# Kernel tuning notes

Hardware: AMD Instinct MI355X
Metric: run time of the kernel (lower is better)

## Reference

```python
import jax, jax.numpy as jnp
import numpy as np

B, N, X, Y, W1, W2, D = 2, 6, 8, 8, 8, 8, 128
H, DH = 4, 32
L = X * Y          # number of windows
QT = N * W1 * W2   # tokens per window
EPS = 1e-5


def _ln(x, g, b):
    m = x.mean(-1, keepdims=True)
    v = ((x - m) ** 2).mean(-1, keepdims=True)
    return (x - m) * jax.lax.rsqrt(v + EPS) * g + b


def _win(t):
    # b n x y w1 w2 d -> b (x y) (n w1 w2) d
    return t.transpose(0, 2, 3, 1, 4, 5, 6).reshape(B, L, QT, D)


def setup_inputs() -> dict:
    key = jax.random.key(0)
    ks = jax.random.split(key, 12)
    s = 0.02
    inp = {
        'q': jax.random.normal(ks[0], (B, N, X, Y, W1, W2, D), jnp.float32),
        'k': jax.random.normal(ks[1], (B, N, X, Y, W1, W2, D), jnp.float32),
        'v': jax.random.normal(ks[2], (B, N, X, Y, W1, W2, D), jnp.float32),
        'skip': jax.random.normal(ks[3], (B, X, Y, W1, W2, D), jnp.float32),
        'gq': jnp.ones((D,), jnp.float32), 'betq': jnp.zeros((D,), jnp.float32),
        'gk': jnp.ones((D,), jnp.float32), 'betk': jnp.zeros((D,), jnp.float32),
        'gv': jnp.ones((D,), jnp.float32), 'betv': jnp.zeros((D,), jnp.float32),
        'wq': jax.random.normal(ks[4], (D, H * DH), jnp.float32) * s,
        'bq': jnp.zeros((H * DH,), jnp.float32),
        'wk': jax.random.normal(ks[5], (D, H * DH), jnp.float32) * s,
        'bk': jnp.zeros((H * DH,), jnp.float32),
        'wv': jax.random.normal(ks[6], (D, H * DH), jnp.float32) * s,
        'bv': jnp.zeros((H * DH,), jnp.float32),
        'wp': jax.random.normal(ks[7], (H * DH, D), jnp.float32) * s,
        'bp': jnp.zeros((D,), jnp.float32),
    }
    return inp


def reference(q, k, v, skip, gq, betq, gk, betk, gv, betv,
              wq, bq, wk, bk, wv, bv, wp, bp):
    scale = DH ** -0.5
    qw, kw, vw = _win(q), _win(k), _win(v)
    # LayerNorm + Linear QKV, split heads: (b, l, T, h, dh)
    qh = (_ln(qw, gq, betq) @ wq + bq).reshape(B, L, QT, H, DH)
    kh = (_ln(kw, gk, betk) @ wk + bk).reshape(B, L, QT, H, DH)
    vh = (_ln(vw, gv, betv) @ wv + bv).reshape(B, L, QT, H, DH)
    dot = scale * jnp.einsum('blqhd,blkhd->bhlqk', qh, kh)
    att = jax.nn.softmax(dot, axis=-1)
    a = jnp.einsum('bhlqk,blkhd->blqhd', att, vh).reshape(B, L, QT, H * DH)
    # b (x y) (n w1 w2) d -> b n x y w1 w2 d
    a = a.reshape(B, X, Y, N, W1, W2, H * DH).transpose(0, 3, 1, 2, 4, 5, 6)
    z = a @ wp + bp
    z = z.mean(1)  # average over views
    return z + skip
```

## Files before the change

### kernel.cpp

```cpp
#include <hip/hip_runtime.h>


typedef unsigned short u16;
typedef __bf16 bf16x8 __attribute__((ext_vector_type(8)));
typedef __bf16 bf16x4 __attribute__((ext_vector_type(4)));
typedef float  f32x16 __attribute__((ext_vector_type(16)));
typedef unsigned short u16x8 __attribute__((ext_vector_type(8)));
typedef unsigned short u16x4 __attribute__((ext_vector_type(4)));

union U8 { u16x8 u; bf16x8 b; u16x4 h[2]; };

#if __has_builtin(__builtin_amdgcn_exp2f)
#define EXP2(x) __builtin_amdgcn_exp2f(x)
#else
#define EXP2(x) exp2f(x)
#endif

__device__ __forceinline__ f32x16 mfma_bf16(bf16x8 a, bf16x8 b, f32x16 c){
  return __builtin_amdgcn_mfma_f32_32x32x16_bf16(a, b, c, 0, 0, 0);
}


__global__ __launch_bounds__(512) void k_prep(
    const float* __restrict__ wq, const float* __restrict__ bq,
    const float* __restrict__ gq, const float* __restrict__ betq,
    const float* __restrict__ wk, const float* __restrict__ bk,
    const float* __restrict__ gk, const float* __restrict__ betk,
    const float* __restrict__ wv, const float* __restrict__ bv,
    const float* __restrict__ gv, const float* __restrict__ betv,
    const float* __restrict__ wp,
    u16* __restrict__ wqT, u16* __restrict__ wkT, u16* __restrict__ wvT, u16* __restrict__ wpT,
    float* __restrict__ bq2, float* __restrict__ bk2, float* __restrict__ bv2,
    float* __restrict__ uq2, float* __restrict__ uk2, float* __restrict__ uv2)
{
  __shared__ float wls[128*33];
  __shared__ float gls[128], bls[128];
  __shared__ float redb[128], redu[128];
  const float ALPHA_Q = 0.17677669529663687f * 1.4426950408889634f;
  int bid = blockIdx.x, tid = threadIdx.x;
  int wsel = bid >> 2, chunk = bid & 3;
  const float *w, *bb, *g, *bet; u16* wT; float *b2, *u2; float alpha;
  if (wsel == 0){ w=wq; bb=bq; g=gq; bet=betq; wT=wqT; b2=bq2; u2=uq2; alpha=ALPHA_Q; }
  else if (wsel == 1){ w=wk; bb=bk; g=gk; bet=betk; wT=wkT; b2=bk2; u2=uk2; alpha=1.f; }
  else if (wsel == 2){ w=wv; bb=bv; g=gv; bet=betv; wT=wvT; b2=bv2; u2=uv2; alpha=1.f; }
  else { w=wp; bb=nullptr; g=nullptr; bet=nullptr; wT=wpT; b2=nullptr; u2=nullptr; alpha=1.f; }

  if (tid < 128){
    gls[tid] = g ? g[tid] : 1.f;
    bls[tid] = bet ? bet[tid] : 0.f;
  }
  const float4* w4 = (const float4*)w;
  #pragma unroll
  for (int i = 0; i < 2; i++){
    int idx = tid + i*512;
    int row = idx >> 3, f4c = idx & 7;
    float4 x = w4[row*32 + chunk*8 + f4c];
    wls[row*33 + f4c*4 + 0] = x.x;
    wls[row*33 + f4c*4 + 1] = x.y;
    wls[row*33 + f4c*4 + 2] = x.z;
    wls[row*33 + f4c*4 + 3] = x.w;
  }
  __syncthreads();
  if (tid < 128){
    int nl = tid >> 2, qp = tid & 3;
    float sb = 0.f, su = 0.f;
    alignas(16) __bf16 tmp[32];
    #pragma unroll
    for (int kk = 0; kk < 32; kk++){
      int k2 = qp*32 + kk;
      float wv_ = wls[k2*33 + nl];
      float gv_ = gls[k2];
      sb += bls[k2] * wv_;
      su += gv_ * wv_;
      tmp[kk] = (__bf16)(wv_ * gv_ * alpha);
    }
    int n = chunk*32 + nl;
    #pragma unroll
    for (int j = 0; j < 4; j++)
      *(bf16x8*)(wT + n*128 + qp*32 + j*8) = *(bf16x8*)&tmp[j*8];
    redb[tid] = sb; redu[tid] = su;
  }
  __syncthreads();
  if (tid < 128){
    int nl = tid >> 2, qp = tid & 3;
    if (qp == 0 && bb){
      int n = chunk*32 + nl;
      float s = bb[n] + redb[tid] + redb[tid+1] + redb[tid+2] + redb[tid+3];
      float u = redu[tid] + redu[tid+1] + redu[tid+2] + redu[tid+3];
      b2[n] = s * alpha;
      u2[n] = u * alpha;
    }
  }
}

__global__ __launch_bounds__(256) void k_lnproj(
    const float* __restrict__ qg, const float* __restrict__ kg, const float* __restrict__ vg,
    const u16* __restrict__ wqT, const u16* __restrict__ wkT, const u16* __restrict__ wvT,
    const float* __restrict__ bq2, const float* __restrict__ bk2, const float* __restrict__ bv2,
    const float* __restrict__ uq2, const float* __restrict__ uk2, const float* __restrict__ uv2,
    u16* __restrict__ qh, u16* __restrict__ kh, u16* __restrict__ vh)
{
  __shared__ alignas(16) u16 Abf[64*136];
  __shared__ float s1s[64], s2s[64];
  int bid = blockIdx.x, tid = threadIdx.x;
  int which = bid % 3;
  int t = bid / 3;
  int n = t % 6, bl = t / 6;
  const float* src; const u16* wT; const float *b2, *u2; u16* dstb;
  if (which == 0){ src=qg; wT=wqT; b2=bq2; u2=uq2; dstb=qh; }
  else if (which == 1){ src=kg; wT=wkT; b2=bk2; u2=uk2; dstb=kh; }
  else { src=vg; wT=wvT; b2=bv2; u2=uv2; dstb=vh; }
  int b = bl >> 6, l = bl & 63;
  const float4* s4 = (const float4*)(src + (size_t)((b*6 + n)*64 + l)*64*128);
  int row = tid >> 2, j = tid & 3;
  float s1 = 0.f, s2 = 0.f;
  #pragma unroll
  for (int i = 0; i < 8; i++){
    float4 xv = s4[row*32 + i*4 + j];
    s1 += xv.x + xv.y + xv.z + xv.w;
    s2 += xv.x*xv.x + xv.y*xv.y + xv.z*xv.z + xv.w*xv.w;
    bf16x4 pk;
    pk[0] = (__bf16)xv.x; pk[1] = (__bf16)xv.y;
    pk[2] = (__bf16)xv.z; pk[3] = (__bf16)xv.w;
    *(bf16x4*)&Abf[row*136 + (i*4 + j)*4] = pk;
  }
  s1 += __shfl_xor(s1, 1, 64); s1 += __shfl_xor(s1, 2, 64);
  s2 += __shfl_xor(s2, 1, 64); s2 += __shfl_xor(s2, 2, 64);
  if (j == 0){
    float m = s1 * (1.f/128.f);
    float r = rsqrtf(s2 * (1.f/128.f) - m*m + 1e-5f);
    s1s[row] = r;
    s2s[row] = r * m;
  }
  __syncthreads();
  int wave = tid >> 6, lane = tid & 63, lm = lane & 31, lh = lane >> 5;
  bf16x8 bfr[8];
  const u16* wrow = wT + (32*wave + lm)*128 + lh*8;
  #pragma unroll
  for (int ks = 0; ks < 8; ks++) bfr[ks] = *(const bf16x8*)(wrow + ks*16);
  f32x16 acc0, acc1;
  #pragma unroll
  for (int r = 0; r < 16; r++){ acc0[r]=0.f; acc1[r]=0.f; }
  #pragma unroll
  for (int ks = 0; ks < 8; ks++){
    bf16x8 a0 = *(const bf16x8*)&Abf[lm*136       + ks*16 + lh*8];
    bf16x8 a1 = *(const bf16x8*)&Abf[(32+lm)*136  + ks*16 + lh*8];
    acc0 = mfma_bf16(a0, bfr[ks], acc0);
    acc1 = mfma_bf16(a1, bfr[ks], acc1);
  }
  int col = 32*wave + lm;
  float u2c = u2[col], bc = b2[col];
  u16* dst = dstb + ((size_t)(bl*4 + wave)*384 + n*64)*32 + lm;
  #pragma unroll
  for (int r = 0; r < 16; r++){
    int row0 = (r&3) + 8*(r>>2) + 4*lh;
    float y0 = s1s[row0]     * acc0[r] - s2s[row0]     * u2c + bc;
    float y1 = s1s[row0+32]  * acc1[r] - s2s[row0+32]  * u2c + bc;
    *(__bf16*)&dst[(size_t)row0*32]      = (__bf16)y0;
    *(__bf16*)&dst[(size_t)(32+row0)*32] = (__bf16)y1;
  }
}

__global__ __launch_bounds__(384) void k_attn(
    const u16* __restrict__ qh, const u16* __restrict__ kh, const u16* __restrict__ vh,
    u16* __restrict__ abar)
{
  __shared__ alignas(16) u16 vts[32*392];
  __shared__ float abar_s[64*32];
  int bid = blockIdx.x, tid = threadIdx.x;
  int h = bid & 3, bl = bid >> 2;
  const u16* qb = qh + (size_t)bid * (384*32);
  const u16* kb = kh + (size_t)bid * (384*32);
  const u16* vb = vh + (size_t)bid * (384*32);

  int wave = tid >> 6, lane = tid & 63, lm = lane & 31, lh = lane >> 5;
  int n = wave;

  const u16* qbase = qb + (size_t)(n*64 + lm)*32 + lh*8;
  bf16x8 qfA0 = *(const bf16x8*)(qbase);
  bf16x8 qfA1 = *(const bf16x8*)(qbase + 16);
  bf16x8 qfB0 = *(const bf16x8*)(qbase + 32*32);
  bf16x8 qfB1 = *(const bf16x8*)(qbase + 32*32 + 16);

  #pragma unroll
  for (int i = 0; i < 4; i++){
    int c = tid + i*384;
    int key = c >> 2, part = c & 3;
    int u = key & 31, tt = key >> 5;
    int a = u >> 2;
    int anew = (a & 4) | ((a & 1) << 1) | ((a >> 1) & 1);
    int pos = tt*32 + anew*4 + (u & 3);
    u16x8 vv = *(const u16x8*)(vb + key*32 + part*8);
    #pragma unroll
    for (int jj = 0; jj < 8; jj++) vts[(part*8 + jj)*392 + pos] = vv[jj];
  }
  for (int idx = tid; idx < 2048; idx += 384) abar_s[idx] = 0.f;
  __syncthreads();

  const u16* vrow = &vts[lm*392 + 8*lh];
  const u16* krow = kb + lm*32 + lh*8;

  bf16x8 ones;
  #pragma unroll
  for (int j = 0; j < 8; j++) ones[j] = (__bf16)1.0f;

  f32x16 oA, oB, slA, slB;
  #pragma unroll
  for (int r = 0; r < 16; r++){ oA[r]=0.f; oB[r]=0.f; slA[r]=0.f; slB[r]=0.f; }

  #pragma unroll
  for (int kt = 0; kt < 12; kt++){
    bf16x8 kf0 = *(const bf16x8*)(krow + kt*1024);
    bf16x8 kf1 = *(const bf16x8*)(krow + kt*1024 + 16);
    f32x16 sa, sb_;
    #pragma unroll
    for (int r = 0; r < 16; r++){ sa[r] = 0.f; sb_[r] = 0.f; }
    __builtin_amdgcn_s_setprio(1);
    sa  = mfma_bf16(kf0, qfA0, sa);
    sb_ = mfma_bf16(kf0, qfB0, sb_);
    sa  = mfma_bf16(kf1, qfA1, sa);
    sb_ = mfma_bf16(kf1, qfB1, sb_);
    __builtin_amdgcn_s_setprio(0);
    U8 v0, v1;
    v0.u = *(const u16x8*)(vrow + kt*32);
    v1.u = *(const u16x8*)(vrow + kt*32 + 16);
    U8 pA0, pA1, pB0, pB1;
    #pragma unroll
    for (int r = 0; r < 8; r++){
      pA0.b[r] = (__bf16)EXP2(sa[r]);
      pA1.b[r] = (__bf16)EXP2(sa[r+8]);
      pB0.b[r] = (__bf16)EXP2(sb_[r]);
      pB1.b[r] = (__bf16)EXP2(sb_[r+8]);
    }
    __builtin_amdgcn_s_setprio(1);
    oA  = mfma_bf16(pA0.b, v0.b, oA);
    oB  = mfma_bf16(pB0.b, v0.b, oB);
    slA = mfma_bf16(pA0.b, ones, slA);
    slB = mfma_bf16(pB0.b, ones, slB);
    oA  = mfma_bf16(pA1.b, v1.b, oA);
    oB  = mfma_bf16(pB1.b, v1.b, oB);
    slA = mfma_bf16(pA1.b, ones, slA);
    slB = mfma_bf16(pB1.b, ones, slB);
    __builtin_amdgcn_s_setprio(0);
  }

  #pragma unroll
  for (int r = 0; r < 16; r++){
    int q_l = (r&3) + 8*(r>>2) + 4*lh;
    float ia = (1.f/6.f) * __builtin_amdgcn_rcpf(slA[r]);
    float ib = (1.f/6.f) * __builtin_amdgcn_rcpf(slB[r]);
    atomicAdd(&abar_s[q_l*32 + lm], oA[r]*ia);
    atomicAdd(&abar_s[(32 + q_l)*32 + lm], oB[r]*ib);
  }
  __syncthreads();
  u16* ob = abar + (size_t)(bl*64)*128 + h*32;
  for (int idx = tid; idx < 2048; idx += 384){
    int w12 = idx >> 5, dh = idx & 31;
    *(__bf16*)&ob[(size_t)w12*128 + dh] = (__bf16)abar_s[idx];
  }
}

__global__ __launch_bounds__(256) void k_out(
    const u16* __restrict__ abar, const u16* __restrict__ wpT,
    const float* __restrict__ bp, const float* __restrict__ skip,
    float* __restrict__ out)
{
  __shared__ alignas(16) u16 Als[32*136];
  int tid = threadIdx.x;
  int R0 = blockIdx.x * 32;
  #pragma unroll
  for (int i = 0; i < 2; i++){
    int c = tid + i*256;
    int row = c >> 4, part = c & 15;
    *(u16x8*)&Als[row*136 + part*8] = *(const u16x8*)(abar + (size_t)(R0+row)*128 + part*8);
  }
  __syncthreads();
  int wave = tid >> 6, lane = tid & 63, lm = lane & 31, lh = lane >> 5;
  bf16x8 bfr[8];
  const u16* wrow = wpT + (32*wave + lm)*128 + lh*8;
  #pragma unroll
  for (int ks = 0; ks < 8; ks++) bfr[ks] = *(const bf16x8*)(wrow + ks*16);
  f32x16 acc;
  #pragma unroll
  for (int r = 0; r < 16; r++) acc[r] = 0.f;
  #pragma unroll
  for (int ks = 0; ks < 8; ks++){
    bf16x8 a0 = *(const bf16x8*)&Als[lm*136 + ks*16 + lh*8];
    acc = mfma_bf16(a0, bfr[ks], acc);
  }
  float bias = bp[32*wave + lm];
  #pragma unroll
  for (int r = 0; r < 16; r++){
    int row0 = (r&3) + 8*(r>>2) + 4*lh;
    size_t f0 = (size_t)(R0 + row0)*128 + 32*wave + lm;
    out[f0] = acc[r] + bias + skip[f0];
  }
}

extern "C" void kernel_launch(void* const* d_in, const int* in_sizes, int n_in,
                              void* d_out, int out_size, void* d_ws, size_t ws_size,
                              hipStream_t stream)
{
  const float* q    = (const float*)d_in[0];
  const float* k    = (const float*)d_in[1];
  const float* v    = (const float*)d_in[2];
  const float* skip = (const float*)d_in[3];
  const float* gq   = (const float*)d_in[4];
  const float* betq = (const float*)d_in[5];
  const float* gk   = (const float*)d_in[6];
  const float* betk = (const float*)d_in[7];
  const float* gv   = (const float*)d_in[8];
  const float* betv = (const float*)d_in[9];
  const float* wq   = (const float*)d_in[10];
  const float* bq   = (const float*)d_in[11];
  const float* wk   = (const float*)d_in[12];
  const float* bk   = (const float*)d_in[13];
  const float* wv   = (const float*)d_in[14];
  const float* bv   = (const float*)d_in[15];
  const float* wp   = (const float*)d_in[16];
  const float* bp   = (const float*)d_in[17];
  float* out = (float*)d_out;

  char* ws = (char*)d_ws;
  u16* wqT = (u16*)ws;
  u16* wkT = wqT + 16384;
  u16* wvT = wkT + 16384;
  u16* wpT = wvT + 16384;
  float* bq2 = (float*)(ws + 131072);
  float* bk2 = bq2 + 128;
  float* bv2 = bk2 + 128;
  float* uq2 = bv2 + 128;
  float* uk2 = uq2 + 128;
  float* uv2 = uk2 + 128;
  u16* qh = (u16*)(ws + 134144);
  u16* kh = qh + 6291456;
  u16* vh = kh + 6291456;
  u16* abar = vh + 6291456;

  k_prep  <<<16,   512, 0, stream>>>(wq,bq,gq,betq, wk,bk,gk,betk, wv,bv,gv,betv, wp,
                                     wqT,wkT,wvT,wpT, bq2,bk2,bv2, uq2,uk2,uv2);
  k_lnproj<<<2304, 256, 0, stream>>>(q,k,v, wqT,wkT,wvT, bq2,bk2,bv2, uq2,uk2,uv2, qh,kh,vh);
  k_attn  <<<512,  384, 0, stream>>>(qh,kh,vh, abar);
  k_out   <<<256,  256, 0, stream>>>(abar, wpT, bp, skip, out);
}
```

Before: 205.9 us.

## Fuse prep, LN-projection, attention and output kernels into one persistent kernel

Replaces the four separate launches (weight prep, LayerNorm+QKV projection, windowed attention, output projection) with one persistent kernel of 512 blocks. The stages are separated by a software grid barrier built on agent-scope atomics, and the barrier counters are reset in rotation. The projection stage is remapped so each 512-thread block runs two 256-thread slots over three passes. The aim is to remove inter-kernel launch gaps and tail effects. The cost is spin-wait barriers, a dependence on all blocks being co-resident, and idle waves in the attention and output stages.

```diff
diff --git a/kernel.cpp b/kernel.cpp
--- a/kernel.cpp
+++ b/kernel.cpp
@@ -20,280 +20,314 @@
   return __builtin_amdgcn_mfma_f32_32x32x16_bf16(a, b, c, 0, 0, 0);
 }
 
-
-__global__ __launch_bounds__(512) void k_prep(
+#define NBLK 512
+
+__device__ int g_bar[3];
+
+__device__ __forceinline__ void grid_sync(int idx){
+  __threadfence();
+  __syncthreads();
+  if (threadIdx.x == 0){
+    int prev = __hip_atomic_fetch_add(&g_bar[idx], 1, __ATOMIC_ACQ_REL,
+                                      __HIP_MEMORY_SCOPE_AGENT);
+    if (prev == NBLK - 1)
+      __hip_atomic_store(&g_bar[(idx+2)%3], 0, __ATOMIC_RELAXED,
+                         __HIP_MEMORY_SCOPE_AGENT);
+    while (__hip_atomic_load(&g_bar[idx], __ATOMIC_ACQUIRE,
+                             __HIP_MEMORY_SCOPE_AGENT) < NBLK)
+      __builtin_amdgcn_s_sleep(2);
+  }
+  __syncthreads();
+}
+
+
+__global__ __launch_bounds__(512, 4) void k_fused(
+    const float* __restrict__ q, const float* __restrict__ k,
+    const float* __restrict__ v, const float* __restrict__ skip,
+    const float* __restrict__ gq, const float* __restrict__ betq,
+    const float* __restrict__ gk, const float* __restrict__ betk,
+    const float* __restrict__ gv, const float* __restrict__ betv,
     const float* __restrict__ wq, const float* __restrict__ bq,
-    const float* __restrict__ gq, const float* __restrict__ betq,
     const float* __restrict__ wk, const float* __restrict__ bk,
-    const float* __restrict__ gk, const float* __restrict__ betk,
     const float* __restrict__ wv, const float* __restrict__ bv,
-    const float* __restrict__ gv, const float* __restrict__ betv,
-    const float* __restrict__ wp,
-    u16* __restrict__ wqT, u16* __restrict__ wkT, u16* __restrict__ wvT, u16* __restrict__ wpT,
+    const float* __restrict__ wp, const float* __restrict__ bp,
+    float* __restrict__ out,
+    u16* __restrict__ wqT, u16* __restrict__ wkT, u16* __restrict__ wvT,
+    u16* __restrict__ wpT,
     float* __restrict__ bq2, float* __restrict__ bk2, float* __restrict__ bv2,
-    float* __restrict__ uq2, float* __restrict__ uk2, float* __restrict__ uv2)
-{
-  __shared__ float wls[128*33];
-  __shared__ float gls[128], bls[128];
-  __shared__ float redb[128], redu[128];
-  const float ALPHA_Q = 0.17677669529663687f * 1.4426950408889634f;
-  int bid = blockIdx.x, tid = threadIdx.x;
-  int wsel = bid >> 2, chunk = bid & 3;
-  const float *w, *bb, *g, *bet; u16* wT; float *b2, *u2; float alpha;
-  if (wsel == 0){ w=wq; bb=bq; g=gq; bet=betq; wT=wqT; b2=bq2; u2=uq2; alpha=ALPHA_Q; }
-  else if (wsel == 1){ w=wk; bb=bk; g=gk; bet=betk; wT=wkT; b2=bk2; u2=uk2; alpha=1.f; }
-  else if (wsel == 2){ w=wv; bb=bv; g=gv; bet=betv; wT=wvT; b2=bv2; u2=uv2; alpha=1.f; }
-  else { w=wp; bb=nullptr; g=nullptr; bet=nullptr; wT=wpT; b2=nullptr; u2=nullptr; alpha=1.f; }
-
-  if (tid < 128){
-    gls[tid] = g ? g[tid] : 1.f;
-    bls[tid] = bet ? bet[tid] : 0.f;
-  }
-  const float4* w4 = (const float4*)w;
-  #pragma unroll
-  for (int i = 0; i < 2; i++){
-    int idx = tid + i*512;
-    int row = idx >> 3, f4c = idx & 7;
-    float4 x = w4[row*32 + chunk*8 + f4c];
-    wls[row*33 + f4c*4 + 0] = x.x;
-    wls[row*33 + f4c*4 + 1] = x.y;
-    wls[row*33 + f4c*4 + 2] = x.z;
-    wls[row*33 + f4c*4 + 3] = x.w;
-  }
-  __syncthreads();
-  if (tid < 128){
-    int nl = tid >> 2, qp = tid & 3;
-    float sb = 0.f, su = 0.f;
-    alignas(16) __bf16 tmp[32];
-    #pragma unroll
-    for (int kk = 0; kk < 32; kk++){
-      int k2 = qp*32 + kk;
-      float wv_ = wls[k2*33 + nl];
-      float gv_ = gls[k2];
-      sb += bls[k2] * wv_;
-      su += gv_ * wv_;
-      tmp[kk] = (__bf16)(wv_ * gv_ * alpha);
-    }
-    int n = chunk*32 + nl;
-    #pragma unroll
-    for (int j = 0; j < 4; j++)
-      *(bf16x8*)(wT + n*128 + qp*32 + j*8) = *(bf16x8*)&tmp[j*8];
-    redb[tid] = sb; redu[tid] = su;
-  }
-  __syncthreads();
-  if (tid < 128){
-    int nl = tid >> 2, qp = tid & 3;
-    if (qp == 0 && bb){
-      int n = chunk*32 + nl;
-      float s = bb[n] + redb[tid] + redb[tid+1] + redb[tid+2] + redb[tid+3];
-      float u = redu[tid] + redu[tid+1] + redu[tid+2] + redu[tid+3];
-      b2[n] = s * alpha;
-      u2[n] = u * alpha;
-    }
-  }
-}
-
-__global__ __launch_bounds__(256) void k_lnproj(
-    const float* __restrict__ qg, const float* __restrict__ kg, const float* __restrict__ vg,
-    const u16* __restrict__ wqT, const u16* __restrict__ wkT, const u16* __restrict__ wvT,
-    const float* __restrict__ bq2, const float* __restrict__ bk2, const float* __restrict__ bv2,
-    const float* __restrict__ uq2, const float* __restrict__ uk2, const float* __restrict__ uv2,
-    u16* __restrict__ qh, u16* __restrict__ kh, u16* __restrict__ vh)
-{
-  __shared__ alignas(16) u16 Abf[64*136];
-  __shared__ float s1s[64], s2s[64];
-  int bid = blockIdx.x, tid = threadIdx.x;
-  int which = bid % 3;
-  int t = bid / 3;
-  int n = t % 6, bl = t / 6;
-  const float* src; const u16* wT; const float *b2, *u2; u16* dstb;
-  if (which == 0){ src=qg; wT=wqT; b2=bq2; u2=uq2; dstb=qh; }
-  else if (which == 1){ src=kg; wT=wkT; b2=bk2; u2=uk2; dstb=kh; }
-  else { src=vg; wT=wvT; b2=bv2; u2=uv2; dstb=vh; }
-  int b = bl >> 6, l = bl & 63;
-  const float4* s4 = (const float4*)(src + (size_t)((b*6 + n)*64 + l)*64*128);
-  int row = tid >> 2, j = tid & 3;
-  float s1 = 0.f, s2 = 0.f;
-  #pragma unroll
-  for (int i = 0; i < 8; i++){
-    float4 xv = s4[row*32 + i*4 + j];
-    s1 += xv.x + xv.y + xv.z + xv.w;
-    s2 += xv.x*xv.x + xv.y*xv.y + xv.z*xv.z + xv.w*xv.w;
-    bf16x4 pk;
-    pk[0] = (__bf16)xv.x; pk[1] = (__bf16)xv.y;
-    pk[2] = (__bf16)xv.z; pk[3] = (__bf16)xv.w;
-    *(bf16x4*)&Abf[row*136 + (i*4 + j)*4] = pk;
-  }
-  s1 += __shfl_xor(s1, 1, 64); s1 += __shfl_xor(s1, 2, 64);
-  s2 += __shfl_xor(s2, 1, 64); s2 += __shfl_xor(s2, 2, 64);
-  if (j == 0){
-    float m = s1 * (1.f/128.f);
-    float r = rsqrtf(s2 * (1.f/128.f) - m*m + 1e-5f);
-    s1s[row] = r;
-    s2s[row] = r * m;
-  }
-  __syncthreads();
-  int wave = tid >> 6, lane = tid & 63, lm = lane & 31, lh = lane >> 5;
-  bf16x8 bfr[8];
-  const u16* wrow = wT + (32*wave + lm)*128 + lh*8;
-  #pragma unroll
-  for (int ks = 0; ks < 8; ks++) bfr[ks] = *(const bf16x8*)(wrow + ks*16);
-  f32x16 acc0, acc1;
-  #pragma unroll
-  for (int r = 0; r < 16; r++){ acc0[r]=0.f; acc1[r]=0.f; }
-  #pragma unroll
-  for (int ks = 0; ks < 8; ks++){
-    bf16x8 a0 = *(const bf16x8*)&Abf[lm*136       + ks*16 + lh*8];
-    bf16x8 a1 = *(const bf16x8*)&Abf[(32+lm)*136  + ks*16 + lh*8];
-    acc0 = mfma_bf16(a0, bfr[ks], acc0);
-    acc1 = mfma_bf16(a1, bfr[ks], acc1);
-  }
-  int col = 32*wave + lm;
-  float u2c = u2[col], bc = b2[col];
-  u16* dst = dstb + ((size_t)(bl*4 + wave)*384 + n*64)*32 + lm;
-  #pragma unroll
-  for (int r = 0; r < 16; r++){
-    int row0 = (r&3) + 8*(r>>2) + 4*lh;
-    float y0 = s1s[row0]     * acc0[r] - s2s[row0]     * u2c + bc;
-    float y1 = s1s[row0+32]  * acc1[r] - s2s[row0+32]  * u2c + bc;
-    *(__bf16*)&dst[(size_t)row0*32]      = (__bf16)y0;
-    *(__bf16*)&dst[(size_t)(32+row0)*32] = (__bf16)y1;
-  }
-}
-
-__global__ __launch_bounds__(384) void k_attn(
-    const u16* __restrict__ qh, const u16* __restrict__ kh, const u16* __restrict__ vh,
+    float* __restrict__ uq2, float* __restrict__ uk2, float* __restrict__ uv2,
+    u16* __restrict__ qh, u16* __restrict__ kh, u16* __restrict__ vh,
     u16* __restrict__ abar)
 {
-  __shared__ alignas(16) u16 vts[32*392];
-  __shared__ float abar_s[64*32];
-  int bid = blockIdx.x, tid = threadIdx.x;
-  int h = bid & 3, bl = bid >> 2;
-  const u16* qb = qh + (size_t)bid * (384*32);
-  const u16* kb = kh + (size_t)bid * (384*32);
-  const u16* vb = vh + (size_t)bid * (384*32);
-
-  int wave = tid >> 6, lane = tid & 63, lm = lane & 31, lh = lane >> 5;
-  int n = wave;
-
-  const u16* qbase = qb + (size_t)(n*64 + lm)*32 + lh*8;
-  bf16x8 qfA0 = *(const bf16x8*)(qbase);
-  bf16x8 qfA1 = *(const bf16x8*)(qbase + 16);
-  bf16x8 qfB0 = *(const bf16x8*)(qbase + 32*32);
-  bf16x8 qfB1 = *(const bf16x8*)(qbase + 32*32 + 16);
-
-  #pragma unroll
-  for (int i = 0; i < 4; i++){
-    int c = tid + i*384;
-    int key = c >> 2, part = c & 3;
-    int u = key & 31, tt = key >> 5;
-    int a = u >> 2;
-    int anew = (a & 4) | ((a & 1) << 1) | ((a >> 1) & 1);
-    int pos = tt*32 + anew*4 + (u & 3);
-    u16x8 vv = *(const u16x8*)(vb + key*32 + part*8);
+  __shared__ __align__(16) char smem[35840];
+  int tid = threadIdx.x;
+
+  if (blockIdx.x < 16){
+    float* wls  = (float*)smem;
+    float* gls  = (float*)(smem + 16896);
+    float* bls  = (float*)(smem + 17408);
+    float* redb = (float*)(smem + 17920);
+    float* redu = (float*)(smem + 18432);
+    const float ALPHA_Q = 0.17677669529663687f * 1.4426950408889634f;
+    int wsel = blockIdx.x >> 2, chunk = blockIdx.x & 3;
+    const float *w, *bb, *g, *bet; u16* wT; float *b2, *u2; float alpha;
+    if (wsel == 0){ w=wq; bb=bq; g=gq; bet=betq; wT=wqT; b2=bq2; u2=uq2; alpha=ALPHA_Q; }
+    else if (wsel == 1){ w=wk; bb=bk; g=gk; bet=betk; wT=wkT; b2=bk2; u2=uk2; alpha=1.f; }
+    else if (wsel == 2){ w=wv; bb=bv; g=gv; bet=betv; wT=wvT; b2=bv2; u2=uv2; alpha=1.f; }
+    else { w=wp; bb=nullptr; g=nullptr; bet=nullptr; wT=wpT; b2=nullptr; u2=nullptr; alpha=1.f; }
+
+    if (tid < 128){
+      gls[tid] = g ? g[tid] : 1.f;
+      bls[tid] = bet ? bet[tid] : 0.f;
+    }
+    const float4* w4 = (const float4*)w;
     #pragma unroll
-    for (int jj = 0; jj < 8; jj++) vts[(part*8 + jj)*392 + pos] = vv[jj];
-  }
-  for (int idx = tid; idx < 2048; idx += 384) abar_s[idx] = 0.f;
-  __syncthreads();
-
-  const u16* vrow = &vts[lm*392 + 8*lh];
-  const u16* krow = kb + lm*32 + lh*8;
-
-  bf16x8 ones;
-  #pragma unroll
-  for (int j = 0; j < 8; j++) ones[j] = (__bf16)1.0f;
-
-  f32x16 oA, oB, slA, slB;
-  #pragma unroll
-  for (int r = 0; r < 16; r++){ oA[r]=0.f; oB[r]=0.f; slA[r]=0.f; slB[r]=0.f; }
-
-  #pragma unroll
-  for (int kt = 0; kt < 12; kt++){
-    bf16x8 kf0 = *(const bf16x8*)(krow + kt*1024);
-    bf16x8 kf1 = *(const bf16x8*)(krow + kt*1024 + 16);
-    f32x16 sa, sb_;
-    #pragma unroll
-    for (int r = 0; r < 16; r++){ sa[r] = 0.f; sb_[r] = 0.f; }
-    __builtin_amdgcn_s_setprio(1);
-    sa  = mfma_bf16(kf0, qfA0, sa);
-    sb_ = mfma_bf16(kf0, qfB0, sb_);
-    sa  = mfma_bf16(kf1, qfA1, sa);
-    sb_ = mfma_bf16(kf1, qfB1, sb_);
-    __builtin_amdgcn_s_setprio(0);
-    U8 v0, v1;
-    v0.u = *(const u16x8*)(vrow + kt*32);
-    v1.u = *(const u16x8*)(vrow + kt*32 + 16);
-    U8 pA0, pA1, pB0, pB1;
-    #pragma unroll
-    for (int r = 0; r < 8; r++){
-      pA0.b[r] = (__bf16)EXP2(sa[r]);
-      pA1.b[r] = (__bf16)EXP2(sa[r+8]);
-      pB0.b[r] = (__bf16)EXP2(sb_[r]);
-      pB1.b[r] = (__bf16)EXP2(sb_[r+8]);
-    }
-    __builtin_amdgcn_s_setprio(1);
-    oA  = mfma_bf16(pA0.b, v0.b, oA);
-    oB  = mfma_bf16(pB0.b, v0.b, oB);
-    slA = mfma_bf16(pA0.b, ones, slA);
-    slB = mfma_bf16(pB0.b, ones, slB);
-    oA  = mfma_bf16(pA1.b, v1.b, oA);
-    oB  = mfma_bf16(pB1.b, v1.b, oB);
-    slA = mfma_bf16(pA1.b, ones, slA);
-    slB = mfma_bf16(pB1.b, ones, slB);
-    __builtin_amdgcn_s_setprio(0);
-  }
-
-  #pragma unroll
-  for (int r = 0; r < 16; r++){
-    int q_l = (r&3) + 8*(r>>2) + 4*lh;
-    float ia = (1.f/6.f) * __builtin_amdgcn_rcpf(slA[r]);
-    float ib = (1.f/6.f) * __builtin_amdgcn_rcpf(slB[r]);
-    atomicAdd(&abar_s[q_l*32 + lm], oA[r]*ia);
-    atomicAdd(&abar_s[(32 + q_l)*32 + lm], oB[r]*ib);
-  }
-  __syncthreads();
-  u16* ob = abar + (size_t)(bl*64)*128 + h*32;
-  for (int idx = tid; idx < 2048; idx += 384){
-    int w12 = idx >> 5, dh = idx & 31;
-    *(__bf16*)&ob[(size_t)w12*128 + dh] = (__bf16)abar_s[idx];
-  }
-}
-
-__global__ __launch_bounds__(256) void k_out(
-    const u16* __restrict__ abar, const u16* __restrict__ wpT,
-    const float* __restrict__ bp, const float* __restrict__ skip,
-    float* __restrict__ out)
-{
-  __shared__ alignas(16) u16 Als[32*136];
-  int tid = threadIdx.x;
-  int R0 = blockIdx.x * 32;
-  #pragma unroll
-  for (int i = 0; i < 2; i++){
-    int c = tid + i*256;
-    int row = c >> 4, part = c & 15;
-    *(u16x8*)&Als[row*136 + part*8] = *(const u16x8*)(abar + (size_t)(R0+row)*128 + part*8);
-  }
-  __syncthreads();
-  int wave = tid >> 6, lane = tid & 63, lm = lane & 31, lh = lane >> 5;
-  bf16x8 bfr[8];
-  const u16* wrow = wpT + (32*wave + lm)*128 + lh*8;
-  #pragma unroll
-  for (int ks = 0; ks < 8; ks++) bfr[ks] = *(const bf16x8*)(wrow + ks*16);
-  f32x16 acc;
-  #pragma unroll
-  for (int r = 0; r < 16; r++) acc[r] = 0.f;
-  #pragma unroll
-  for (int ks = 0; ks < 8; ks++){
-    bf16x8 a0 = *(const bf16x8*)&Als[lm*136 + ks*16 + lh*8];
-    acc = mfma_bf16(a0, bfr[ks], acc);
-  }
-  float bias = bp[32*wave + lm];
-  #pragma unroll
-  for (int r = 0; r < 16; r++){
-    int row0 = (r&3) + 8*(r>>2) + 4*lh;
-    size_t f0 = (size_t)(R0 + row0)*128 + 32*wave + lm;
-    out[f0] = acc[r] + bias + skip[f0];
+    for (int i = 0; i < 2; i++){
+      int idx = tid + i*512;
+      int row = idx >> 3, f4c = idx & 7;
+      float4 x = w4[row*32 + chunk*8 + f4c];
+      wls[row*33 + f4c*4 + 0] = x.x;
+      wls[row*33 + f4c*4 + 1] = x.y;
+      wls[row*33 + f4c*4 + 2] = x.z;
+      wls[row*33 + f4c*4 + 3] = x.w;
+    }
+    __syncthreads();
+    if (tid < 128){
+      int nl = tid >> 2, qp = tid & 3;
+      float sb = 0.f, su = 0.f;
+      alignas(16) __bf16 tmp[32];
+      #pragma unroll
+      for (int kk = 0; kk < 32; kk++){
+        int k2 = qp*32 + kk;
+        float wv_ = wls[k2*33 + nl];
+        float gv_ = gls[k2];
+        sb += bls[k2] * wv_;
+        su += gv_ * wv_;
+        tmp[kk] = (__bf16)(wv_ * gv_ * alpha);
+      }
+      int n = chunk*32 + nl;
+      #pragma unroll
+      for (int j = 0; j < 4; j++)
+        *(bf16x8*)(wT + n*128 + qp*32 + j*8) = *(bf16x8*)&tmp[j*8];
+      redb[tid] = sb; redu[tid] = su;
+    }
+    __syncthreads();
+    if (tid < 128){
+      int nl = tid >> 2, qp = tid & 3;
+      if (qp == 0 && bb){
+        int n = chunk*32 + nl;
+        float s = bb[n] + redb[tid] + redb[tid+1] + redb[tid+2] + redb[tid+3];
+        float u = redu[tid] + redu[tid+1] + redu[tid+2] + redu[tid+3];
+        b2[n] = s * alpha;
+        u2[n] = u * alpha;
+      }
+    }
+  }
+  grid_sync(0);
+
+  {
+    int slot = tid >> 8, t2 = tid & 255;
+    int base = blockIdx.x + slot*512;
+    char* sm = smem + slot*17920;
+    u16* Abf   = (u16*)sm;
+    float* s1s = (float*)(sm + 17408);
+    float* s2s = (float*)(sm + 17664);
+    #pragma unroll 1
+    for (int r = 0; r < 3; ++r){
+      bool act = base < 768;
+      int task = base*3 + r;
+      int which = r;
+      int n = base % 6, bl = (base / 6) & 127;
+      const float* src; const u16* wT; const float *b2, *u2; u16* dstb;
+      if (which == 0){ src=q; wT=wqT; b2=bq2; u2=uq2; dstb=qh; }
+      else if (which == 1){ src=k; wT=wkT; b2=bk2; u2=uk2; dstb=kh; }
+      else { src=v; wT=wvT; b2=bv2; u2=uv2; dstb=vh; }
+      (void)task;
+      int b = bl >> 6, l = bl & 63;
+      const float4* s4 = (const float4*)(src + (size_t)((b*6 + n)*64 + l)*64*128);
+      int row = t2 >> 2, j = t2 & 3;
+      float s1 = 0.f, s2 = 0.f;
+      if (act){
+        #pragma unroll
+        for (int i = 0; i < 8; i++){
+          float4 xv = s4[row*32 + i*4 + j];
+          s1 += xv.x + xv.y + xv.z + xv.w;
+          s2 += xv.x*xv.x + xv.y*xv.y + xv.z*xv.z + xv.w*xv.w;
+          bf16x4 pk;
+          pk[0] = (__bf16)xv.x; pk[1] = (__bf16)xv.y;
+          pk[2] = (__bf16)xv.z; pk[3] = (__bf16)xv.w;
+          *(bf16x4*)&Abf[row*136 + (i*4 + j)*4] = pk;
+        }
+      }
+      s1 += __shfl_xor(s1, 1, 64); s1 += __shfl_xor(s1, 2, 64);
+      s2 += __shfl_xor(s2, 1, 64); s2 += __shfl_xor(s2, 2, 64);
+      if (act && j == 0){
+        float m = s1 * (1.f/128.f);
+        float rr = rsqrtf(s2 * (1.f/128.f) - m*m + 1e-5f);
+        s1s[row] = rr;
+        s2s[row] = rr * m;
+      }
+      __syncthreads();
+      if (act){
+        int wv2 = (tid >> 6) & 3, lane = tid & 63, lm = lane & 31, lh = lane >> 5;
+        bf16x8 bfr[8];
+        const u16* wrow = wT + (32*wv2 + lm)*128 + lh*8;
+        #pragma unroll
+        for (int ks = 0; ks < 8; ks++) bfr[ks] = *(const bf16x8*)(wrow + ks*16);
+        f32x16 acc0, acc1;
+        #pragma unroll
+        for (int rr2 = 0; rr2 < 16; rr2++){ acc0[rr2]=0.f; acc1[rr2]=0.f; }
+        #pragma unroll
+        for (int ks = 0; ks < 8; ks++){
+          bf16x8 a0 = *(const bf16x8*)&Abf[lm*136       + ks*16 + lh*8];
+          bf16x8 a1 = *(const bf16x8*)&Abf[(32+lm)*136  + ks*16 + lh*8];
+          acc0 = mfma_bf16(a0, bfr[ks], acc0);
+          acc1 = mfma_bf16(a1, bfr[ks], acc1);
+        }
+        int col = 32*wv2 + lm;
+        float u2c = u2[col], bc = b2[col];
+        u16* dst = dstb + ((size_t)(bl*4 + wv2)*384 + n*64)*32 + lm;
+        #pragma unroll
+        for (int rr2 = 0; rr2 < 16; rr2++){
+          int row0 = (rr2&3) + 8*(rr2>>2) + 4*lh;
+          float y0 = s1s[row0]     * acc0[rr2] - s2s[row0]     * u2c + bc;
+          float y1 = s1s[row0+32]  * acc1[rr2] - s2s[row0+32]  * u2c + bc;
+          *(__bf16*)&dst[(size_t)row0*32]      = (__bf16)y0;
+          *(__bf16*)&dst[(size_t)(32+row0)*32] = (__bf16)y1;
+        }
+      }
+      __syncthreads();
+    }
+  }
+  grid_sync(1);
+
+  {
+    u16* vts     = (u16*)smem;
+    float* abar_s = (float*)(smem + 25088);
+    int bid2 = blockIdx.x;
+    int h = bid2 & 3, bl = bid2 >> 2;
+    const u16* qb = qh + (size_t)bid2 * 12288;
+    const u16* kb = kh + (size_t)bid2 * 12288;
+    const u16* vb = vh + (size_t)bid2 * 12288;
+    int wave = tid >> 6, lane = tid & 63, lm = lane & 31, lh = lane >> 5;
+
+    bf16x8 qfA0, qfA1, qfB0, qfB1;
+    if (wave < 6){
+      const u16* qbase = qb + (size_t)(wave*64 + lm)*32 + lh*8;
+      qfA0 = *(const bf16x8*)(qbase);
+      qfA1 = *(const bf16x8*)(qbase + 16);
+      qfB0 = *(const bf16x8*)(qbase + 32*32);
+      qfB1 = *(const bf16x8*)(qbase + 32*32 + 16);
+    }
+    for (int c = tid; c < 1536; c += 512){
+      int key = c >> 2, part = c & 3;
+      int u = key & 31, tt2 = key >> 5;
+      int a = u >> 2;
+      int anew = (a & 4) | ((a & 1) << 1) | ((a >> 1) & 1);
+      int pos = tt2*32 + anew*4 + (u & 3);
+      u16x8 vv = *(const u16x8*)(vb + key*32 + part*8);
+      #pragma unroll
+      for (int jj = 0; jj < 8; jj++) vts[(part*8 + jj)*392 + pos] = vv[jj];
+    }
+    for (int idx = tid; idx < 2048; idx += 512) abar_s[idx] = 0.f;
+    __syncthreads();
+
+    if (wave < 6){
+      int n = wave;
+      (void)n;
+      const u16* vrow = &vts[lm*392 + 8*lh];
+      const u16* krow = kb + lm*32 + lh*8;
+      bf16x8 ones;
+      #pragma unroll
+      for (int j2 = 0; j2 < 8; j2++) ones[j2] = (__bf16)1.0f;
+      f32x16 oA, oB, slA, slB;
+      #pragma unroll
+      for (int r2 = 0; r2 < 16; r2++){ oA[r2]=0.f; oB[r2]=0.f; slA[r2]=0.f; slB[r2]=0.f; }
+      #pragma unroll
+      for (int kt = 0; kt < 12; kt++){
+        bf16x8 kf0 = *(const bf16x8*)(krow + kt*1024);
+        bf16x8 kf1 = *(const bf16x8*)(krow + kt*1024 + 16);
+        f32x16 sa, sb_;
+        #pragma unroll
+        for (int r2 = 0; r2 < 16; r2++){ sa[r2] = 0.f; sb_[r2] = 0.f; }
+        __builtin_amdgcn_s_setprio(1);
+        sa  = mfma_bf16(kf0, qfA0, sa);
+        sb_ = mfma_bf16(kf0, qfB0, sb_);
+        sa  = mfma_bf16(kf1, qfA1, sa);
+        sb_ = mfma_bf16(kf1, qfB1, sb_);
+        __builtin_amdgcn_s_setprio(0);
+        U8 v0, v1;
+        v0.u = *(const u16x8*)(vrow + kt*32);
+        v1.u = *(const u16x8*)(vrow + kt*32 + 16);
+        U8 pA0, pA1, pB0, pB1;
+        #pragma unroll
+        for (int r2 = 0; r2 < 8; r2++){
+          pA0.b[r2] = (__bf16)EXP2(sa[r2]);
+          pA1.b[r2] = (__bf16)EXP2(sa[r2+8]);
+          pB0.b[r2] = (__bf16)EXP2(sb_[r2]);
+          pB1.b[r2] = (__bf16)EXP2(sb_[r2+8]);
+        }
+        __builtin_amdgcn_s_setprio(1);
+        oA  = mfma_bf16(pA0.b, v0.b, oA);
+        oB  = mfma_bf16(pB0.b, v0.b, oB);
+        slA = mfma_bf16(pA0.b, ones, slA);
+        slB = mfma_bf16(pB0.b, ones, slB);
+        oA  = mfma_bf16(pA1.b, v1.b, oA);
+        oB  = mfma_bf16(pB1.b, v1.b, oB);
+        slA = mfma_bf16(pA1.b, ones, slA);
+        slB = mfma_bf16(pB1.b, ones, slB);
+        __builtin_amdgcn_s_setprio(0);
+      }
+      #pragma unroll
+      for (int r2 = 0; r2 < 16; r2++){
+        int q_l = (r2&3) + 8*(r2>>2) + 4*lh;
+        float ia = (1.f/6.f) * __builtin_amdgcn_rcpf(slA[r2]);
+        float ib = (1.f/6.f) * __builtin_amdgcn_rcpf(slB[r2]);
+        atomicAdd(&abar_s[q_l*32 + lm], oA[r2]*ia);
+        atomicAdd(&abar_s[(32 + q_l)*32 + lm], oB[r2]*ib);
+      }
+    }
+    __syncthreads();
+    u16* ob = abar + (size_t)(bl*64)*128 + h*32;
+    for (int idx = tid; idx < 2048; idx += 512){
+      int w12 = idx >> 5, dh = idx & 31;
+      *(__bf16*)&ob[(size_t)w12*128 + dh] = (__bf16)abar_s[idx];
+    }
+  }
+  grid_sync(2);
+
+  if (blockIdx.x < 256){
+    u16* Als = (u16*)smem;
+    int R0 = blockIdx.x * 32;
+    {
+      int c = tid;
+      int row = c >> 4, part = c & 15;
+      *(u16x8*)&Als[row*136 + part*8] =
+          *(const u16x8*)(abar + (size_t)(R0+row)*128 + part*8);
+    }
+    __syncthreads();
+    if (tid < 256){
+      int wave = tid >> 6, lane = tid & 63, lm = lane & 31, lh = lane >> 5;
+      bf16x8 bfr[8];
+      const u16* wrow = wpT + (32*wave + lm)*128 + lh*8;
+      #pragma unroll
+      for (int ks = 0; ks < 8; ks++) bfr[ks] = *(const bf16x8*)(wrow + ks*16);
+      f32x16 acc;
+      #pragma unroll
+      for (int r2 = 0; r2 < 16; r2++) acc[r2] = 0.f;
+      #pragma unroll
+      for (int ks = 0; ks < 8; ks++){
+        bf16x8 a0 = *(const bf16x8*)&Als[lm*136 + ks*16 + lh*8];
+        acc = mfma_bf16(a0, bfr[ks], acc);
+      }
+      float bias = bp[32*wave + lm];
+      #pragma unroll
+      for (int r2 = 0; r2 < 16; r2++){
+        int row0 = (r2&3) + 8*(r2>>2) + 4*lh;
+        size_t f0 = (size_t)(R0 + row0)*128 + 32*wave + lm;
+        out[f0] = acc[r2] + bias + skip[f0];
+      }
+    }
   }
 }
 
@@ -337,9 +371,9 @@
   u16* vh = kh + 6291456;
   u16* abar = vh + 6291456;
 
-  k_prep  <<<16,   512, 0, stream>>>(wq,bq,gq,betq, wk,bk,gk,betk, wv,bv,gv,betv, wp,
-                                     wqT,wkT,wvT,wpT, bq2,bk2,bv2, uq2,uk2,uv2);
-  k_lnproj<<<2304, 256, 0, stream>>>(q,k,v, wqT,wkT,wvT, bq2,bk2,bv2, uq2,uk2,uv2, qh,kh,vh);
-  k_attn  <<<512,  384, 0, stream>>>(qh,kh,vh, abar);
-  k_out   <<<256,  256, 0, stream>>>(abar, wpT, bp, skip, out);
+  k_fused<<<NBLK, 512, 0, stream>>>(
+      q, k, v, skip, gq, betq, gk, betk, gv, betv,
+      wq, bq, wk, bk, wv, bv, wp, bp, out,
+      wqT, wkT, wvT, wpT, bq2, bk2, bv2, uq2, uk2, uv2,
+      qh, kh, vh, abar);
 }
```

Measured after the change: 603.1 us. 2.93x slower.

## Split attention blocks across view halves and stage projection stores through LDS

Applied to the files above, without the earlier changes.

The attention kernel now launches twice as many blocks of 192 threads. Each block handles three of the six views and writes fp32 partial view-sums into one of two buffers, which the output kernel adds together before its projection. The aim is more parallelism and occupancy on the attention stage. Separately, the projection kernel now stages its bf16 outputs in shared memory and writes them with coalesced 16-byte stores instead of scattered 2-byte stores. The cost is that each block now loads the full V tile for only half the queries, and the intermediate fp32 traffic is larger.

```diff
diff --git a/kernel.cpp b/kernel.cpp
--- a/kernel.cpp
+++ b/kernel.cpp
@@ -150,31 +150,41 @@
   }
   int col = 32*wave + lm;
   float u2c = u2[col], bc = b2[col];
-  u16* dst = dstb + ((size_t)(bl*4 + wave)*384 + n*64)*32 + lm;
+  __syncthreads();
   #pragma unroll
   for (int r = 0; r < 16; r++){
     int row0 = (r&3) + 8*(r>>2) + 4*lh;
     float y0 = s1s[row0]     * acc0[r] - s2s[row0]     * u2c + bc;
     float y1 = s1s[row0+32]  * acc1[r] - s2s[row0+32]  * u2c + bc;
-    *(__bf16*)&dst[(size_t)row0*32]      = (__bf16)y0;
-    *(__bf16*)&dst[(size_t)(32+row0)*32] = (__bf16)y1;
-  }
-}
-
-__global__ __launch_bounds__(384) void k_attn(
+    *(__bf16*)&Abf[row0*136 + col]      = (__bf16)y0;
+    *(__bf16*)&Abf[(32+row0)*136 + col] = (__bf16)y1;
+  }
+  __syncthreads();
+  #pragma unroll
+  for (int i = 0; i < 4; i++){
+    int c = tid + i*256;
+    int grp = c >> 8, rw = (c >> 2) & 63, part = c & 3;
+    u16x8 val = *(const u16x8*)&Abf[rw*136 + grp*32 + part*8];
+    *(u16x8*)(dstb + ((size_t)(bl*4 + grp)*384 + n*64 + rw)*32 + part*8) = val;
+  }
+}
+
+__global__ __launch_bounds__(192) void k_attn(
     const u16* __restrict__ qh, const u16* __restrict__ kh, const u16* __restrict__ vh,
-    u16* __restrict__ abar)
+    float* __restrict__ abp0, float* __restrict__ abp1)
 {
   __shared__ alignas(16) u16 vts[32*392];
   __shared__ float abar_s[64*32];
   int bid = blockIdx.x, tid = threadIdx.x;
-  int h = bid & 3, bl = bid >> 2;
-  const u16* qb = qh + (size_t)bid * (384*32);
-  const u16* kb = kh + (size_t)bid * (384*32);
-  const u16* vb = vh + (size_t)bid * (384*32);
+  int g = bid & 1;
+  int bh = bid >> 1;
+  int h = bh & 3, bl = bh >> 2;
+  const u16* qb = qh + (size_t)bh * 12288;
+  const u16* kb = kh + (size_t)bh * 12288;
+  const u16* vb = vh + (size_t)bh * 12288;
 
   int wave = tid >> 6, lane = tid & 63, lm = lane & 31, lh = lane >> 5;
-  int n = wave;
+  int n = g*3 + wave;
 
   const u16* qbase = qb + (size_t)(n*64 + lm)*32 + lh*8;
   bf16x8 qfA0 = *(const bf16x8*)(qbase);
@@ -183,8 +193,8 @@
   bf16x8 qfB1 = *(const bf16x8*)(qbase + 32*32 + 16);
 
   #pragma unroll
-  for (int i = 0; i < 4; i++){
-    int c = tid + i*384;
+  for (int i = 0; i < 8; i++){
+    int c = tid + i*192;
     int key = c >> 2, part = c & 3;
     int u = key & 31, tt = key >> 5;
     int a = u >> 2;
@@ -194,7 +204,7 @@
     #pragma unroll
     for (int jj = 0; jj < 8; jj++) vts[(part*8 + jj)*392 + pos] = vv[jj];
   }
-  for (int idx = tid; idx < 2048; idx += 384) abar_s[idx] = 0.f;
+  for (int idx = tid; idx < 2048; idx += 192) abar_s[idx] = 0.f;
   __syncthreads();
 
   const u16* vrow = &vts[lm*392 + 8*lh];
@@ -253,15 +263,16 @@
     atomicAdd(&abar_s[(32 + q_l)*32 + lm], oB[r]*ib);
   }
   __syncthreads();
-  u16* ob = abar + (size_t)(bl*64)*128 + h*32;
-  for (int idx = tid; idx < 2048; idx += 384){
+  float* ob = (g ? abp1 : abp0) + (size_t)(bl*64)*128 + h*32;
+  for (int idx = tid; idx < 2048; idx += 192){
     int w12 = idx >> 5, dh = idx & 31;
-    *(__bf16*)&ob[(size_t)w12*128 + dh] = (__bf16)abar_s[idx];
+    ob[(size_t)w12*128 + dh] = abar_s[idx];
   }
 }
 
 __global__ __launch_bounds__(256) void k_out(
-    const u16* __restrict__ abar, const u16* __restrict__ wpT,
+    const float* __restrict__ abp0, const float* __restrict__ abp1,
+    const u16* __restrict__ wpT,
     const float* __restrict__ bp, const float* __restrict__ skip,
     float* __restrict__ out)
 {
@@ -269,10 +280,15 @@
   int tid = threadIdx.x;
   int R0 = blockIdx.x * 32;
   #pragma unroll
-  for (int i = 0; i < 2; i++){
+  for (int i = 0; i < 4; i++){
     int c = tid + i*256;
-    int row = c >> 4, part = c & 15;
-    *(u16x8*)&Als[row*136 + part*8] = *(const u16x8*)(abar + (size_t)(R0+row)*128 + part*8);
+    int rw = c >> 5, part = c & 31;
+    float4 a = ((const float4*)(abp0 + (size_t)(R0+rw)*128))[part];
+    float4 b = ((const float4*)(abp1 + (size_t)(R0+rw)*128))[part];
+    bf16x4 pk;
+    pk[0] = (__bf16)(a.x + b.x); pk[1] = (__bf16)(a.y + b.y);
+    pk[2] = (__bf16)(a.z + b.z); pk[3] = (__bf16)(a.w + b.w);
+    *(bf16x4*)&Als[rw*136 + part*4] = pk;
   }
   __syncthreads();
   int wave = tid >> 6, lane = tid & 63, lm = lane & 31, lh = lane >> 5;
@@ -335,11 +351,12 @@
   u16* qh = (u16*)(ws + 134144);
   u16* kh = qh + 6291456;
   u16* vh = kh + 6291456;
-  u16* abar = vh + 6291456;
+  float* abp0 = (float*)(ws + 37882880);
+  float* abp1 = abp0 + 1048576;
 
   k_prep  <<<16,   512, 0, stream>>>(wq,bq,gq,betq, wk,bk,gk,betk, wv,bv,gv,betv, wp,
                                      wqT,wkT,wvT,wpT, bq2,bk2,bv2, uq2,uk2,uv2);
   k_lnproj<<<2304, 256, 0, stream>>>(q,k,v, wqT,wkT,wvT, bq2,bk2,bv2, uq2,uk2,uv2, qh,kh,vh);
-  k_attn  <<<512,  384, 0, stream>>>(qh,kh,vh, abar);
-  k_out   <<<256,  256, 0, stream>>>(abar, wpT, bp, skip, out);
-}
+  k_attn  <<<1024, 192, 0, stream>>>(qh,kh,vh, abp0,abp1);
+  k_out   <<<256,  256, 0, stream>>>(abp0,abp1, wpT, bp, skip, out);
+}
```

After: 219.1 us. +6.4%, slower.

## Compute softmax denominators with VALU sums, prefetch K, stage projection stores through LDS

Applied to the files above, without the earlier changes.

In the attention kernel, the softmax row sums are now accumulated from the fp32 exponentials in registers, with a cross-lane shuffle reduction. This replaces the extra MFMAs against a ones vector and halves the matrix work in the PV phase. All K fragments are preloaded into registers before the V transpose, and the V LDS row pitch is changed, presumably to reduce bank conflicts. The projection kernel now writes its bf16 outputs to LDS and then does coalesced 16-byte global stores instead of scattered 2-byte stores. The costs are much higher register pressure from 24 K fragments, the shuffles, and an extra barrier.

```diff
diff --git a/kernel.cpp b/kernel.cpp
--- a/kernel.cpp
+++ b/kernel.cpp
@@ -150,14 +150,22 @@
   }
   int col = 32*wave + lm;
   float u2c = u2[col], bc = b2[col];
-  u16* dst = dstb + ((size_t)(bl*4 + wave)*384 + n*64)*32 + lm;
+  __syncthreads();
   #pragma unroll
   for (int r = 0; r < 16; r++){
     int row0 = (r&3) + 8*(r>>2) + 4*lh;
     float y0 = s1s[row0]     * acc0[r] - s2s[row0]     * u2c + bc;
     float y1 = s1s[row0+32]  * acc1[r] - s2s[row0+32]  * u2c + bc;
-    *(__bf16*)&dst[(size_t)row0*32]      = (__bf16)y0;
-    *(__bf16*)&dst[(size_t)(32+row0)*32] = (__bf16)y1;
+    *(__bf16*)&Abf[row0*136 + col]      = (__bf16)y0;
+    *(__bf16*)&Abf[(32+row0)*136 + col] = (__bf16)y1;
+  }
+  __syncthreads();
+  #pragma unroll
+  for (int i = 0; i < 4; i++){
+    int c = tid + i*256;
+    int grp = c >> 8, rw = (c >> 2) & 63, part = c & 3;
+    u16x8 val = *(const u16x8*)&Abf[rw*136 + grp*32 + part*8];
+    *(u16x8*)(dstb + ((size_t)(bl*4 + grp)*384 + n*64 + rw)*32 + part*8) = val;
   }
 }
 
@@ -165,7 +173,7 @@
     const u16* __restrict__ qh, const u16* __restrict__ kh, const u16* __restrict__ vh,
     u16* __restrict__ abar)
 {
-  __shared__ alignas(16) u16 vts[32*392];
+  __shared__ alignas(16) u16 vts[32*408];
   __shared__ float abar_s[64*32];
   int bid = blockIdx.x, tid = threadIdx.x;
   int h = bid & 3, bl = bid >> 2;
@@ -181,6 +189,15 @@
   bf16x8 qfA1 = *(const bf16x8*)(qbase + 16);
   bf16x8 qfB0 = *(const bf16x8*)(qbase + 32*32);
   bf16x8 qfB1 = *(const bf16x8*)(qbase + 32*32 + 16);
+
+  const u16* krow = kb + lm*32 + lh*8;
+  bf16x8 kfr[24];
+  #pragma unroll
+  for (int kt = 0; kt < 12; kt++){
+    kfr[2*kt]   = *(const bf16x8*)(krow + kt*1024);
+    kfr[2*kt+1] = *(const bf16x8*)(krow + kt*1024 + 16);
+  }
+  __builtin_amdgcn_sched_barrier(0);
 
   #pragma unroll
   for (int i = 0; i < 4; i++){
@@ -192,26 +209,22 @@
     int pos = tt*32 + anew*4 + (u & 3);
     u16x8 vv = *(const u16x8*)(vb + key*32 + part*8);
     #pragma unroll
-    for (int jj = 0; jj < 8; jj++) vts[(part*8 + jj)*392 + pos] = vv[jj];
+    for (int jj = 0; jj < 8; jj++) vts[(part*8 + jj)*408 + pos] = vv[jj];
   }
   for (int idx = tid; idx < 2048; idx += 384) abar_s[idx] = 0.f;
   __syncthreads();
 
-  const u16* vrow = &vts[lm*392 + 8*lh];
-  const u16* krow = kb + lm*32 + lh*8;
-
-  bf16x8 ones;
-  #pragma unroll
-  for (int j = 0; j < 8; j++) ones[j] = (__bf16)1.0f;
-
-  f32x16 oA, oB, slA, slB;
-  #pragma unroll
-  for (int r = 0; r < 16; r++){ oA[r]=0.f; oB[r]=0.f; slA[r]=0.f; slB[r]=0.f; }
+  const u16* vrow = &vts[lm*408 + 8*lh];
+
+  f32x16 oA, oB;
+  #pragma unroll
+  for (int r = 0; r < 16; r++){ oA[r] = 0.f; oB[r] = 0.f; }
+  float sleA = 0.f, sleB = 0.f;
 
   #pragma unroll
   for (int kt = 0; kt < 12; kt++){
-    bf16x8 kf0 = *(const bf16x8*)(krow + kt*1024);
-    bf16x8 kf1 = *(const bf16x8*)(krow + kt*1024 + 16);
+    bf16x8 kf0 = kfr[2*kt];
+    bf16x8 kf1 = kfr[2*kt+1];
     f32x16 sa, sb_;
     #pragma unroll
     for (int r = 0; r < 16; r++){ sa[r] = 0.f; sb_[r] = 0.f; }
@@ -227,30 +240,37 @@
     U8 pA0, pA1, pB0, pB1;
     #pragma unroll
     for (int r = 0; r < 8; r++){
-      pA0.b[r] = (__bf16)EXP2(sa[r]);
-      pA1.b[r] = (__bf16)EXP2(sa[r+8]);
-      pB0.b[r] = (__bf16)EXP2(sb_[r]);
-      pB1.b[r] = (__bf16)EXP2(sb_[r+8]);
+      float eA0 = EXP2(sa[r]);
+      float eA1 = EXP2(sa[r+8]);
+      float eB0 = EXP2(sb_[r]);
+      float eB1 = EXP2(sb_[r+8]);
+      sleA += eA0 + eA1;
+      sleB += eB0 + eB1;
+      pA0.b[r] = (__bf16)eA0;
+      pA1.b[r] = (__bf16)eA1;
+      pB0.b[r] = (__bf16)eB0;
+      pB1.b[r] = (__bf16)eB1;
     }
     __builtin_amdgcn_s_setprio(1);
-    oA  = mfma_bf16(pA0.b, v0.b, oA);
-    oB  = mfma_bf16(pB0.b, v0.b, oB);
-    slA = mfma_bf16(pA0.b, ones, slA);
-    slB = mfma_bf16(pB0.b, ones, slB);
-    oA  = mfma_bf16(pA1.b, v1.b, oA);
-    oB  = mfma_bf16(pB1.b, v1.b, oB);
-    slA = mfma_bf16(pA1.b, ones, slA);
-    slB = mfma_bf16(pB1.b, ones, slB);
+    oA = mfma_bf16(pA0.b, v0.b, oA);
+    oB = mfma_bf16(pB0.b, v0.b, oB);
+    oA = mfma_bf16(pA1.b, v1.b, oA);
+    oB = mfma_bf16(pB1.b, v1.b, oB);
     __builtin_amdgcn_s_setprio(0);
   }
+
+  sleA += __shfl_xor(sleA, 32, 64);
+  sleB += __shfl_xor(sleB, 32, 64);
+  float invA = (1.f/6.f) / sleA;
+  float invB = (1.f/6.f) / sleB;
 
   #pragma unroll
   for (int r = 0; r < 16; r++){
     int q_l = (r&3) + 8*(r>>2) + 4*lh;
-    float ia = (1.f/6.f) * __builtin_amdgcn_rcpf(slA[r]);
-    float ib = (1.f/6.f) * __builtin_amdgcn_rcpf(slB[r]);
-    atomicAdd(&abar_s[q_l*32 + lm], oA[r]*ia);
-    atomicAdd(&abar_s[(32 + q_l)*32 + lm], oB[r]*ib);
+    float a = oA[r] * __shfl(invA, q_l, 64);
+    float b = oB[r] * __shfl(invB, q_l, 64);
+    atomicAdd(&abar_s[q_l*32 + lm], a);
+    atomicAdd(&abar_s[(32 + q_l)*32 + lm], b);
   }
   __syncthreads();
   u16* ob = abar + (size_t)(bl*64)*128 + h*32;
```

Result: no change. 208.3 us (+1.2%).
